# Kernel tuning notes

Measured on AMD Instinct MI355X. Metric: run time of the kernel, lower is better.

The kernel has to match this reference:

```python
import jax, jax.numpy as jnp
import numpy as np

N_NODES = 100000
N_EDGES = 500000
D = 256
EPS = 0.1  # GIN epsilon applied on self-loop relation


def setup_inputs() -> dict:
    key = jax.random.key(0)
    ks = jax.random.split(key, 9)
    return {
        "x": jax.random.normal(ks[0], (N_NODES, D), dtype=jnp.float32),
        "W_self": jax.random.normal(ks[1], (D, D), dtype=jnp.float32) * 0.05,
        "W_r1": jax.random.normal(ks[2], (D, D), dtype=jnp.float32) * 0.05,
        "W_r2": jax.random.normal(ks[3], (D, D), dtype=jnp.float32) * 0.05,
        "bias": jax.random.normal(ks[4], (D,), dtype=jnp.float32) * 0.05,
        "src1": jax.random.randint(ks[5], (N_EDGES,), 0, N_NODES, dtype=jnp.int32),
        "dst1": jax.random.randint(ks[6], (N_EDGES,), 0, N_NODES, dtype=jnp.int32),
        "src2": jax.random.randint(ks[7], (N_EDGES,), 0, N_NODES, dtype=jnp.int32),
        "dst2": jax.random.randint(ks[8], (N_EDGES,), 0, N_NODES, dtype=jnp.int32),
    }


def reference(x, W_self, W_r1, W_r2, bias, src1, dst1, src2, dst2):
    # self-loop relation: features scaled by (1+eps); one self-loop edge per node
    # so copy_u + sum delivers each node exactly its own message.
    h = (1.0 + EPS) * (x @ W_self)
    # regular relations: per-node message = x @ W, gathered along src edges,
    # scatter-summed at dst (DGL fn.copy_u + fn.sum, cross-etype 'sum' reducer).
    msg1 = x @ W_r1
    h = h + jax.ops.segment_sum(msg1[src1], dst1, num_segments=N_NODES)
    msg2 = x @ W_r2
    h = h + jax.ops.segment_sum(msg2[src2], dst2, num_segments=N_NODES)
    # bias + activation, then second activation (applied twice in original);
    # mlp/batch_norm are None, dropout is identity in eval.
    h = jax.nn.relu(h + bias)
    h = jax.nn.relu(h)
    return h
```

## Files before the change

### kernel.cpp

```cpp
#include <hip/hip_runtime.h>

#define N_NODES 100000
#define N_EDGES 500000
#define D 256
#define CAP 32
#define BM 128

typedef __bf16 bf16x8 __attribute__((ext_vector_type(8)));
typedef float  f32x4  __attribute__((ext_vector_type(4)));
typedef unsigned int u32x2 __attribute__((ext_vector_type(2)));

__device__ __forceinline__ unsigned short f2bf(float f) {
    unsigned int u = __float_as_uint(f);
    u += 0x7fffu + ((u >> 16) & 1u);
    return (unsigned short)(u >> 16);
}
__device__ __forceinline__ float bf2f(unsigned short b) {
    return __uint_as_float(((unsigned int)b) << 16);
}

__device__ __forceinline__ void glds16(const unsigned short* g, unsigned short* l) {
    __builtin_amdgcn_global_load_lds(
        (const __attribute__((address_space(1))) unsigned int*)g,
        (__attribute__((address_space(3))) unsigned int*)l,
        16, 0, 0);
}

#define PREP_BLOCKS 17188

__global__ __launch_bounds__(256) void prep_kernel(
    const float* __restrict__ x, unsigned short* __restrict__ xb,
    const float* __restrict__ Ws, const float* __restrict__ W1,
    const float* __restrict__ W2, unsigned short* __restrict__ Wt,
    const int* __restrict__ src1, const int* __restrict__ dst1,
    const int* __restrict__ src2, const int* __restrict__ dst2,
    int* __restrict__ cnt1, int* __restrict__ cnt2,
    int* __restrict__ bkt1, int* __restrict__ bkt2)
{
    const int wid  = blockIdx.x * 4 + (threadIdx.x >> 6);
    const int lane = threadIdx.x & 63;
    const int group = wid / 22;
    const int pos   = wid - group * 22;

    if (pos < 16) {
        int cw = group * 16 + pos;
        if (cw >= 50000) return;
        size_t base = (size_t)cw * 512;
        float4 a = *(const float4*)(x + base + lane * 4);
        float4 c = *(const float4*)(x + base + 256 + lane * 4);
        ushort4 oa, oc;
        oa.x = f2bf(a.x); oa.y = f2bf(a.y); oa.z = f2bf(a.z); oa.w = f2bf(a.w);
        oc.x = f2bf(c.x); oc.y = f2bf(c.y); oc.z = f2bf(c.z); oc.w = f2bf(c.w);
        *(ushort4*)(xb + base + lane * 4) = oa;
        *(ushort4*)(xb + base + 256 + lane * 4) = oc;
    } else if (pos < 21) {
        int bw = group * 5 + (pos - 16);
        int e = bw * 64 + lane;
        if (e >= 2 * N_EDGES) return;
        bool r2 = (e >= N_EDGES);
        const int* src = r2 ? src2 : src1;
        const int* dst = r2 ? dst2 : dst1;
        int* cnt = r2 ? cnt2 : cnt1;
        int* bkt = r2 ? bkt2 : bkt1;
        int ei = r2 ? e - N_EDGES : e;
        int s = src[ei], d = dst[ei];
        int p = atomicAdd(&cnt[d], 1);
        if (p < CAP) bkt[d * CAP + p] = s;
    } else {
        int idx = group * 64 + lane;
        if (idx >= 3 * D * D) return;
        int k = idx >> 8;
        int n = idx & (D - 1);
        const float* W = (k < D) ? Ws : (k < 2 * D ? W1 : W2);
        float scale = (k < D) ? 1.1f : 1.0f;
        int dk = k ^ ((((n >> 1) & 3)) << 3);
        Wt[(size_t)n * (3 * D) + dk] = f2bf(W[(size_t)(k & (D - 1)) * D + n] * scale);
    }
}

__global__ __launch_bounds__(256) void gather_kernel(
    const unsigned short* __restrict__ xb,
    const int* __restrict__ cnt1, const int* __restrict__ cnt2,
    const int* __restrict__ bkt1, const int* __restrict__ bkt2,
    unsigned short* __restrict__ xa1, unsigned short* __restrict__ xa2)
{
    long long gid = (long long)blockIdx.x * blockDim.x + threadIdx.x;
    int node = (int)(gid >> 6);
    int lane = (int)(gid & 63);
    if (node >= N_NODES) return;

    int c1 = cnt1[node]; if (c1 > CAP) c1 = CAP;
    int c2 = cnt2[node]; if (c2 > CAP) c2 = CAP;
    int sid1 = (lane < c1) ? bkt1[(size_t)node * CAP + lane] : 0;
    int sid2 = (lane < c2) ? bkt2[(size_t)node * CAP + lane] : 0;

    ushort4 v1[8], v2[8];
    #pragma unroll
    for (int t = 0; t < 8; ++t)
        v1[t] = *(const ushort4*)(xb + (size_t)__shfl(sid1, t) * D + lane * 4);
    #pragma unroll
    for (int t = 0; t < 8; ++t)
        v2[t] = *(const ushort4*)(xb + (size_t)__shfl(sid2, t) * D + lane * 4);

    {
        float a0 = 0.f, a1 = 0.f, a2 = 0.f, a3 = 0.f;
        #pragma unroll
        for (int t = 0; t < 8; ++t)
            if (t < c1) {
                a0 += bf2f(v1[t].x); a1 += bf2f(v1[t].y);
                a2 += bf2f(v1[t].z); a3 += bf2f(v1[t].w);
            }
        for (int e = 8; e < c1; ++e) {
            int s = __shfl(sid1, e);
            ushort4 t = *(const ushort4*)(xb + (size_t)s * D + lane * 4);
            a0 += bf2f(t.x); a1 += bf2f(t.y); a2 += bf2f(t.z); a3 += bf2f(t.w);
        }
        u32x2 o;
        o.x = (unsigned)f2bf(a0) | ((unsigned)f2bf(a1) << 16);
        o.y = (unsigned)f2bf(a2) | ((unsigned)f2bf(a3) << 16);
        __builtin_nontemporal_store(o, (u32x2*)(xa1 + (size_t)node * D + lane * 4));
    }

    {
        float a0 = 0.f, a1 = 0.f, a2 = 0.f, a3 = 0.f;
        #pragma unroll
        for (int t = 0; t < 8; ++t)
            if (t < c2) {
                a0 += bf2f(v2[t].x); a1 += bf2f(v2[t].y);
                a2 += bf2f(v2[t].z); a3 += bf2f(v2[t].w);
            }
        for (int e = 8; e < c2; ++e) {
            int s = __shfl(sid2, e);
            ushort4 t = *(const ushort4*)(xb + (size_t)s * D + lane * 4);
            a0 += bf2f(t.x); a1 += bf2f(t.y); a2 += bf2f(t.z); a3 += bf2f(t.w);
        }
        u32x2 o;
        o.x = (unsigned)f2bf(a0) | ((unsigned)f2bf(a1) << 16);
        o.y = (unsigned)f2bf(a2) | ((unsigned)f2bf(a3) << 16);
        __builtin_nontemporal_store(o, (u32x2*)(xa2 + (size_t)node * D + lane * 4));
    }
}

__global__ __launch_bounds__(512, 4) void gemm_kernel(
    const unsigned short* __restrict__ xb,
    const unsigned short* __restrict__ xa1,
    const unsigned short* __restrict__ xa2,
    const unsigned short* __restrict__ Wt,
    const float* __restrict__ bias, float* __restrict__ out)
{
    __shared__ unsigned short Alds[2][BM * 32];
    __shared__ unsigned short Blds[2][256 * 32];

    const int tid  = threadIdx.x;
    const int lane = tid & 63;
    const int wave = tid >> 6;
    const int quad = lane >> 4;
    const int l15  = lane & 15;
    const int m0 = blockIdx.x * BM;
    const int wm = (wave >> 2) * 64;
    const int wn = (wave & 3) * 64;
    const int swz = (l15 >> 1) & 3;

    const int gr   = lane >> 2;
    const int gch  = lane & 3;
    const int gswz = (lane >> 3) & 3;
    int mRow = m0 + (wave << 4) + gr;
    if (mRow >= N_NODES) mRow = N_NODES - 1;
    const size_t aRowOff = (size_t)mRow * D + ((gch ^ gswz) << 3);
    const unsigned short* bSrc0 = Wt + (size_t)((wave << 4) + gr) * (3 * D) + (gch << 3);
    const unsigned short* bSrc1 = bSrc0 + (size_t)128 * (3 * D);
    const unsigned short* Aseg[3] = {xb, xa1, xa2};

    f32x4 acc[4][4] = {};

    glds16(Aseg[0] + aRowOff, &Alds[0][wave * 512]);
    glds16(bSrc0, &Blds[0][wave * 512]);
    glds16(bSrc1, &Blds[0][4096 + wave * 512]);
    __syncthreads();

    for (int kt = 0; kt < 24; ++kt) {
        const int ktn = kt + 1;
        if (ktn < 24) {
            glds16(Aseg[ktn >> 3] + aRowOff + ((ktn & 7) * 32), &Alds[ktn & 1][wave * 512]);
            glds16(bSrc0 + ktn * 32, &Blds[ktn & 1][wave * 512]);
            glds16(bSrc1 + ktn * 32, &Blds[ktn & 1][4096 + wave * 512]);
        }

        const unsigned short* Ab = &Alds[kt & 1][0];
        const unsigned short* Bb = &Blds[kt & 1][0];
        bf16x8 b0f = *(const bf16x8*)(Bb + (wn +  0 + l15) * 32 + ((quad ^ swz) * 8));
        bf16x8 b1f = *(const bf16x8*)(Bb + (wn + 16 + l15) * 32 + ((quad ^ swz) * 8));
        bf16x8 b2f = *(const bf16x8*)(Bb + (wn + 32 + l15) * 32 + ((quad ^ swz) * 8));
        bf16x8 b3f = *(const bf16x8*)(Bb + (wn + 48 + l15) * 32 + ((quad ^ swz) * 8));
        #pragma unroll
        for (int i = 0; i < 4; ++i) {
            bf16x8 afi = *(const bf16x8*)(Ab + (wm + i * 16 + l15) * 32 + ((quad ^ swz) * 8));
            acc[i][0] = __builtin_amdgcn_mfma_f32_16x16x32_bf16(afi, b0f, acc[i][0], 0, 0, 0);
            acc[i][1] = __builtin_amdgcn_mfma_f32_16x16x32_bf16(afi, b1f, acc[i][1], 0, 0, 0);
            acc[i][2] = __builtin_amdgcn_mfma_f32_16x16x32_bf16(afi, b2f, acc[i][2], 0, 0, 0);
            acc[i][3] = __builtin_amdgcn_mfma_f32_16x16x32_bf16(afi, b3f, acc[i][3], 0, 0, 0);
        }
        __syncthreads();
    }

    #pragma unroll
    for (int j = 0; j < 4; ++j) {
        int col = wn + j * 16 + l15;
        float bj = bias[col];
        #pragma unroll
        for (int i = 0; i < 4; ++i) {
            int rb = m0 + wm + i * 16 + quad * 4;
            #pragma unroll
            for (int r = 0; r < 4; ++r) {
                int m = rb + r;
                if (m < N_NODES)
                    __builtin_nontemporal_store(
                        fmaxf(acc[i][j][r] + bj, 0.f),
                        out + (size_t)m * D + col);
            }
        }
    }
}

extern "C" void kernel_launch(void* const* d_in, const int* in_sizes, int n_in,
                              void* d_out, int out_size, void* d_ws, size_t ws_size,
                              hipStream_t stream) {
    const float* x    = (const float*)d_in[0];
    const float* Ws   = (const float*)d_in[1];
    const float* W1   = (const float*)d_in[2];
    const float* W2   = (const float*)d_in[3];
    const float* bias = (const float*)d_in[4];
    const int* src1   = (const int*)d_in[5];
    const int* dst1   = (const int*)d_in[6];
    const int* src2   = (const int*)d_in[7];
    const int* dst2   = (const int*)d_in[8];
    float* out = (float*)d_out;

    char* p = (char*)d_ws;
    unsigned short* xb  = (unsigned short*)p; p += (size_t)N_NODES * D * 2;
    unsigned short* xa1 = (unsigned short*)p; p += (size_t)N_NODES * D * 2;
    unsigned short* xa2 = (unsigned short*)p; p += (size_t)N_NODES * D * 2;
    int* cnt1 = (int*)p; p += (size_t)N_NODES * 4;
    int* cnt2 = (int*)p; p += (size_t)N_NODES * 4;
    int* bkt1 = (int*)p; p += (size_t)N_NODES * CAP * 4;
    int* bkt2 = (int*)p; p += (size_t)N_NODES * CAP * 4;
    unsigned short* Wt = (unsigned short*)p;

    (void)hipMemsetAsync(cnt1, 0, (size_t)2 * N_NODES * 4, stream);

    prep_kernel<<<PREP_BLOCKS, 256, 0, stream>>>(
        x, xb, Ws, W1, W2, Wt, src1, dst1, src2, dst2, cnt1, cnt2, bkt1, bkt2);

    {
        long long total = (long long)N_NODES * 64;
        gather_kernel<<<(int)((total + 255) / 256), 256, 0, stream>>>(
            xb, cnt1, cnt2, bkt1, bkt2, xa1, xa2);
    }
    {
        gemm_kernel<<<(N_NODES + BM - 1) / BM, 512, 0, stream>>>(
            xb, xa1, xa2, Wt, bias, out);
    }
}
```

Before: 385.9 us.

## Triple-buffer GEMM LDS tiles with prefetch distance two and explicit vmcnt waits

The GEMM K-loop moves from double to triple buffering in LDS and prefetches two K-tiles ahead. It uses manual s_waitcnt vmcnt counts plus raw s_barrier instead of __syncthreads, so loads for later tiles can stay in flight while the current tile is consumed. The aggregation kernel's stores to xa1/xa2 become normal stores instead of nontemporal ones, so the GEMM can later read them from cache. The cost is 50% more LDS per block, which may lower occupancy, and hand-tuned wait counts that depend on how the compiler counts memory operations.

```diff
diff --git a/kernel.cpp b/kernel.cpp
--- a/kernel.cpp
+++ b/kernel.cpp
@@ -118,7 +118,7 @@
         u32x2 o;
         o.x = (unsigned)f2bf(a0) | ((unsigned)f2bf(a1) << 16);
         o.y = (unsigned)f2bf(a2) | ((unsigned)f2bf(a3) << 16);
-        __builtin_nontemporal_store(o, (u32x2*)(xa1 + (size_t)node * D + lane * 4));
+        *(u32x2*)(xa1 + (size_t)node * D + lane * 4) = o;
     }
 
     {
@@ -137,7 +137,7 @@
         u32x2 o;
         o.x = (unsigned)f2bf(a0) | ((unsigned)f2bf(a1) << 16);
         o.y = (unsigned)f2bf(a2) | ((unsigned)f2bf(a3) << 16);
-        __builtin_nontemporal_store(o, (u32x2*)(xa2 + (size_t)node * D + lane * 4));
+        *(u32x2*)(xa2 + (size_t)node * D + lane * 4) = o;
     }
 }
 
@@ -148,8 +148,8 @@
     const unsigned short* __restrict__ Wt,
     const float* __restrict__ bias, float* __restrict__ out)
 {
-    __shared__ unsigned short Alds[2][BM * 32];
-    __shared__ unsigned short Blds[2][256 * 32];
+    __shared__ unsigned short Alds[3][BM * 32];
+    __shared__ unsigned short Blds[3][256 * 32];
 
     const int tid  = threadIdx.x;
     const int lane = tid & 63;
@@ -173,21 +173,30 @@
 
     f32x4 acc[4][4] = {};
 
-    glds16(Aseg[0] + aRowOff, &Alds[0][wave * 512]);
-    glds16(bSrc0, &Blds[0][wave * 512]);
-    glds16(bSrc1, &Blds[0][4096 + wave * 512]);
-    __syncthreads();
+    glds16(Aseg[0] + aRowOff,            &Alds[0][wave * 512]);
+    glds16(bSrc0,                        &Blds[0][wave * 512]);
+    glds16(bSrc1,                        &Blds[0][4096 + wave * 512]);
+    glds16(Aseg[0] + aRowOff + 32,       &Alds[1][wave * 512]);
+    glds16(bSrc0 + 32,                   &Blds[1][wave * 512]);
+    glds16(bSrc1 + 32,                   &Blds[1][4096 + wave * 512]);
 
     for (int kt = 0; kt < 24; ++kt) {
-        const int ktn = kt + 1;
-        if (ktn < 24) {
-            glds16(Aseg[ktn >> 3] + aRowOff + ((ktn & 7) * 32), &Alds[ktn & 1][wave * 512]);
-            glds16(bSrc0 + ktn * 32, &Blds[ktn & 1][wave * 512]);
-            glds16(bSrc1 + ktn * 32, &Blds[ktn & 1][4096 + wave * 512]);
-        }
-
-        const unsigned short* Ab = &Alds[kt & 1][0];
-        const unsigned short* Bb = &Blds[kt & 1][0];
+        const int kpre = kt + 2;
+        if (kpre < 24) {
+            const int b = kpre % 3;
+            glds16(Aseg[kpre >> 3] + aRowOff + ((kpre & 7) * 32), &Alds[b][wave * 512]);
+            glds16(bSrc0 + kpre * 32, &Blds[b][wave * 512]);
+            glds16(bSrc1 + kpre * 32, &Blds[b][4096 + wave * 512]);
+        }
+
+        if (kt < 22)       asm volatile("s_waitcnt vmcnt(6)" ::: "memory");
+        else if (kt == 22) asm volatile("s_waitcnt vmcnt(3)" ::: "memory");
+        else               asm volatile("s_waitcnt vmcnt(0)" ::: "memory");
+        __builtin_amdgcn_s_barrier();
+        asm volatile("" ::: "memory");
+
+        const unsigned short* Ab = &Alds[kt % 3][0];
+        const unsigned short* Bb = &Blds[kt % 3][0];
         bf16x8 b0f = *(const bf16x8*)(Bb + (wn +  0 + l15) * 32 + ((quad ^ swz) * 8));
         bf16x8 b1f = *(const bf16x8*)(Bb + (wn + 16 + l15) * 32 + ((quad ^ swz) * 8));
         bf16x8 b2f = *(const bf16x8*)(Bb + (wn + 32 + l15) * 32 + ((quad ^ swz) * 8));
@@ -200,7 +209,10 @@
             acc[i][2] = __builtin_amdgcn_mfma_f32_16x16x32_bf16(afi, b2f, acc[i][2], 0, 0, 0);
             acc[i][3] = __builtin_amdgcn_mfma_f32_16x16x32_bf16(afi, b3f, acc[i][3], 0, 0, 0);
         }
-        __syncthreads();
+
+        asm volatile("" ::: "memory");
+        __builtin_amdgcn_s_barrier();
+        asm volatile("" ::: "memory");
     }
 
     #pragma unroll
```

After: 376.8 us. -2.3%, faster.
